# Performance work log

Hardware: AMD Instinct MI355X
Metric: run time of the kernel (lower is better)

## Reference

```python
import jax, jax.numpy as jnp
import numpy as np

B = 4096
N_PATCH = 196  # 14x14 patches of a 28x28 image
THRESHOLD = 0.9
SECONDARY = 0.5
SECONDARY_WEIGHT = 0.5

_CNOT = jnp.array([[1, 0, 0, 0], [0, 1, 0, 0], [0, 0, 0, 1], [0, 0, 1, 0]], dtype=jnp.complex64)


def _ry(t):
    c, s = jnp.cos(t / 2), jnp.sin(t / 2)
    m = jnp.stack([jnp.stack([c, -s], -1), jnp.stack([s, c], -1)], -2)
    return m.astype(jnp.complex64)


def _rx(t):
    c, s = jnp.cos(t / 2), jnp.sin(t / 2)
    z = jnp.zeros_like(c)
    re = jnp.stack([jnp.stack([c, z], -1), jnp.stack([z, c], -1)], -2)
    im = jnp.stack([jnp.stack([z, -s], -1), jnp.stack([-s, z], -1)], -2)
    return (re + 1j * im).astype(jnp.complex64)


def _rz(t):
    em = jnp.exp(-0.5j * t.astype(jnp.complex64) if hasattr(t, 'astype') else -0.5j * t)
    ep = jnp.conj(em)
    z = jnp.zeros_like(em)
    m = jnp.stack([jnp.stack([em, z], -1), jnp.stack([z, ep], -1)], -2)
    return m.astype(jnp.complex64)


def _apply_1q(state, mat, wire):
    # state: (P, 2, 2, 2, 2); mat: (2,2) shared or (P,2,2) per-sample
    s = jnp.moveaxis(state, 1 + wire, -1)
    if mat.ndim == 2:
        s = jnp.einsum('pabcj,ij->pabci', s, mat)
    else:
        s = jnp.einsum('pabcj,pij->pabci', s, mat)
    return jnp.moveaxis(s, -1, 1 + wire)


def _apply_2q(state, mat4, w0, w1):
    s = jnp.moveaxis(state, (1 + w0, 1 + w1), (-2, -1))
    shp = s.shape
    s = s.reshape(shp[:-2] + (4,))
    s = jnp.einsum('...j,ij->...i', s, mat4)
    return jnp.moveaxis(s.reshape(shp), (-2, -1), (1 + w0, 1 + w1))


def _quantum_measure(angles, q_params):
    # angles: (P, 4) real -> Pauli-Z expectations (P, 4)
    P = angles.shape[0]
    state = jnp.zeros((P, 2, 2, 2, 2), jnp.complex64).at[:, 0, 0, 0, 0].set(1.0)
    # GeneralEncoder: RY(pixel) on each wire
    for w in range(4):
        state = _apply_1q(state, _ry(angles[:, w]), w)
    # fixed 'RandomLayer' (8 ops, deterministic gate sequence, trainable params)
    state = _apply_1q(state, _rx(q_params[0]), 0)
    state = _apply_1q(state, _ry(q_params[1]), 1)
    state = _apply_1q(state, _rz(q_params[2]), 2)
    state = _apply_2q(state, _CNOT, 0, 1)
    state = _apply_1q(state, _rx(q_params[3]), 3)
    state = _apply_2q(state, _CNOT, 2, 3)
    state = _apply_1q(state, _ry(q_params[4]), 0)
    state = _apply_1q(state, _rz(q_params[5]), 3)
    probs = state.real ** 2 + state.imag ** 2
    exps = []
    for w in range(4):
        p = jnp.moveaxis(probs, 1 + w, 1)
        exps.append((p[:, 0] - p[:, 1]).reshape(P, -1).sum(-1))
    return jnp.stack(exps, -1)


def setup_inputs() -> dict:
    key = jax.random.key(0)
    k1, k2, k3, k4 = jax.random.split(key, 4)
    x = jax.random.uniform(k1, (B, 1, 28, 28), dtype=jnp.float32)
    q_params = jax.random.uniform(k2, (6,), dtype=jnp.float32) * 2.0 * np.pi
    W = jax.random.normal(k3, (10, 4 * 14 * 14), dtype=jnp.float32) * 0.03
    b = jax.random.normal(k4, (10,), dtype=jnp.float32) * 0.01
    return {"x": x, "q_params": q_params, "W": W, "b": b}


def reference(x, q_params, W, b):
    Bsz = x.shape[0]
    # extract 2x2 patches in (tl, tr, bl, br) order -> (B*196, 4)
    p = x[:, 0].reshape(Bsz, 14, 2, 14, 2)
    p = jnp.transpose(p, (0, 1, 3, 2, 4)).reshape(Bsz * N_PATCH, 4)
    meas = _quantum_measure(p, q_params).reshape(Bsz, N_PATCH, 4)
    # adjacency from cosine similarity of first sample's patch vectors
    v = meas[0]
    nrm = jnp.linalg.norm(v, axis=-1, keepdims=True)
    sim = (v @ v.T) / (nrm * nrm.T + 1e-12)
    adj = jnp.where(sim >= THRESHOLD, 1.0,
                    jnp.where(sim >= SECONDARY, SECONDARY_WEIGHT, 0.0)).astype(meas.dtype)
    agg = jnp.einsum('nm,bmd->bnd', adj, meas)
    logits = agg.reshape(Bsz, -1) @ W.T + b
    return jax.nn.log_softmax(logits, axis=-1)
```

## Files before the change

kernel.cpp:

```cpp
#include <hip/hip_runtime.h>
#include <hip/hip_bf16.h>


#define NP 196

__device__ __forceinline__ float quad3(const float* H, const float* wa,
                                       const float* wb) {
  return wa[0] * (H[0] * wb[0] + H[1] * wb[1] + H[2] * wb[2]) +
         wa[1] * (H[3] * wb[0] + H[4] * wb[1] + H[5] * wb[2]) +
         wa[2] * (H[6] * wb[0] + H[7] * wb[1] + H[8] * wb[2]);
}

__device__ __forceinline__ void build_H_all(const float* __restrict__ qp,
                                            float* __restrict__ H) {
  float qc[6], qs[6];
#pragma unroll
  for (int i = 0; i < 6; ++i) __sincosf(0.5f * qp[i], &qs[i], &qc[i]);
#pragma unroll
  for (int sub = 0; sub < 2; ++sub) {
    float Mr[4][4] = {}, Mi[4][4] = {};
    if (sub == 0) {
      Mr[0][0] = Mr[1][1] = Mr[2][2] = Mr[3][3] = qc[0];
      Mi[0][2] = Mi[2][0] = Mi[1][3] = Mi[3][1] = -qs[0];
#pragma unroll
      for (int j = 0; j < 4; ++j) {
        float a, b;
        a = Mr[0][j]; b = Mr[1][j]; Mr[0][j] = qc[1]*a - qs[1]*b; Mr[1][j] = qs[1]*a + qc[1]*b;
        a = Mi[0][j]; b = Mi[1][j]; Mi[0][j] = qc[1]*a - qs[1]*b; Mi[1][j] = qs[1]*a + qc[1]*b;
        a = Mr[2][j]; b = Mr[3][j]; Mr[2][j] = qc[1]*a - qs[1]*b; Mr[3][j] = qs[1]*a + qc[1]*b;
        a = Mi[2][j]; b = Mi[3][j]; Mi[2][j] = qc[1]*a - qs[1]*b; Mi[3][j] = qs[1]*a + qc[1]*b;
      }
#pragma unroll
      for (int j = 0; j < 4; ++j) {
        float r = Mr[2][j]; Mr[2][j] = Mr[3][j]; Mr[3][j] = r;
        float q = Mi[2][j]; Mi[2][j] = Mi[3][j]; Mi[3][j] = q;
      }
#pragma unroll
      for (int j = 0; j < 4; ++j) {
        float a, b;
        a = Mr[0][j]; b = Mr[2][j]; Mr[0][j] = qc[4]*a - qs[4]*b; Mr[2][j] = qs[4]*a + qc[4]*b;
        a = Mi[0][j]; b = Mi[2][j]; Mi[0][j] = qc[4]*a - qs[4]*b; Mi[2][j] = qs[4]*a + qc[4]*b;
        a = Mr[1][j]; b = Mr[3][j]; Mr[1][j] = qc[4]*a - qs[4]*b; Mr[3][j] = qs[4]*a + qc[4]*b;
        a = Mi[1][j]; b = Mi[3][j]; Mi[1][j] = qc[4]*a - qs[4]*b; Mi[3][j] = qs[4]*a + qc[4]*b;
      }
    } else {
      Mr[0][0] = Mr[1][1] = Mr[2][2] = Mr[3][3] = qc[2];
      Mi[0][0] = Mi[1][1] = -qs[2]; Mi[2][2] = Mi[3][3] = qs[2];
#pragma unroll
      for (int j = 0; j < 4; ++j) {
        float ra, ia, rb, ib;
        ra = Mr[0][j]; ia = Mi[0][j]; rb = Mr[1][j]; ib = Mi[1][j];
        Mr[0][j] = qc[3]*ra + qs[3]*ib;  Mi[0][j] = qc[3]*ia - qs[3]*rb;
        Mr[1][j] = qc[3]*rb + qs[3]*ia;  Mi[1][j] = qc[3]*ib - qs[3]*ra;
        ra = Mr[2][j]; ia = Mi[2][j]; rb = Mr[3][j]; ib = Mi[3][j];
        Mr[2][j] = qc[3]*ra + qs[3]*ib;  Mi[2][j] = qc[3]*ia - qs[3]*rb;
        Mr[3][j] = qc[3]*rb + qs[3]*ia;  Mi[3][j] = qc[3]*ib - qs[3]*ra;
      }
#pragma unroll
      for (int j = 0; j < 4; ++j) {
        float r = Mr[2][j]; Mr[2][j] = Mr[3][j]; Mr[3][j] = r;
        float q = Mi[2][j]; Mi[2][j] = Mi[3][j]; Mi[3][j] = q;
      }
#pragma unroll
      for (int r = 0; r < 4; ++r) {
        float sg = (r & 1) ? 1.0f : -1.0f;
#pragma unroll
        for (int j = 0; j < 4; ++j) {
          float re = Mr[r][j], im = Mi[r][j];
          Mr[r][j] = qc[5] * re - sg * qs[5] * im;
          Mi[r][j] = qc[5] * im + sg * qs[5] * re;
        }
      }
    }
#pragma unroll
    for (int d = 0; d < 2; ++d) {
      float G[4][4];
#pragma unroll
      for (int j = 0; j < 4; ++j)
#pragma unroll
        for (int k = 0; k < 4; ++k) {
          float g = 0.0f;
#pragma unroll
          for (int i = 0; i < 4; ++i) {
            float sg = (d == 0) ? ((i < 2) ? 1.f : -1.f)
                                : (((i & 1) == 0) ? 1.f : -1.f);
            g += sg * (Mr[i][j] * Mr[i][k] + Mi[i][j] * Mi[i][k]);
          }
          G[j][k] = g;
        }
      float* Hd = H + sub * 18 + d * 9;
      Hd[0] = G[0][0];       Hd[1] = 2.f * G[0][1];               Hd[2] = G[1][1];
      Hd[3] = 2.f * G[0][2]; Hd[4] = 2.f * (G[0][3] + G[1][2]);   Hd[5] = 2.f * G[1][3];
      Hd[6] = G[2][2];       Hd[7] = 2.f * G[2][3];               Hd[8] = G[3][3];
    }
  }
}

__device__ __forceinline__ void meas_patch(const float* __restrict__ xb, int p,
                                           const float* __restrict__ H,
                                           float* e) {
  int i = p / 14, j = p - 14 * i;
  float2 top = *(const float2*)(xb + 56 * i + 2 * j);
  float2 bot = *(const float2*)(xb + 56 * i + 28 + 2 * j);
  float c0, s0, c1, s1, c2, s2, c3, s3;
  __sincosf(0.5f * top.x, &s0, &c0);
  __sincosf(0.5f * top.y, &s1, &c1);
  __sincosf(0.5f * bot.x, &s2, &c2);
  __sincosf(0.5f * bot.y, &s3, &c3);
  float wA0[3] = {c0 * c0, c0 * s0, s0 * s0};
  float wA1[3] = {c1 * c1, c1 * s1, s1 * s1};
  float wB0[3] = {c2 * c2, c2 * s2, s2 * s2};
  float wB1[3] = {c3 * c3, c3 * s3, s3 * s3};
  e[0] = quad3(H, wA0, wA1);
  e[1] = quad3(H + 9, wA0, wA1);
  e[2] = quad3(H + 18, wB0, wB1);
  e[3] = quad3(H + 27, wB0, wB1);
}

__global__ __launch_bounds__(256, 1) void k_w2(const float* __restrict__ x,
                                               const float* __restrict__ qp,
                                               const float* __restrict__ W,
                                               float* __restrict__ W2,
                                               float* __restrict__ HG) {
  __shared__ float vs[NP][4];
  __shared__ float ns[NP];
  __shared__ float wrow[NP];
  __shared__ float red[160];
  int m = blockIdx.x, t = threadIdx.x;

  float H[36];
  build_H_all(qp, H);

  if (m == 0 && t == 0) {
#pragma unroll
    for (int i = 0; i < 36; ++i) HG[i] = H[i];
  }

  if (t < NP) {
    float e[4];
    meas_patch(x, t, H, e);
    vs[t][0] = e[0]; vs[t][1] = e[1]; vs[t][2] = e[2]; vs[t][3] = e[3];
    ns[t] = sqrtf(e[0]*e[0] + e[1]*e[1] + e[2]*e[2] + e[3]*e[3]);
  }
  __syncthreads();
  float v0 = vs[m][0], v1 = vs[m][1], v2 = vs[m][2], v3 = vs[m][3];
  float nm = ns[m];
  if (t < NP) {
    float dot = v0 * vs[t][0] + v1 * vs[t][1] + v2 * vs[t][2] + v3 * vs[t][3];
    float sim = dot / (nm * ns[t] + 1e-12f);
    wrow[t] = (sim >= 0.9f) ? 1.0f : ((sim >= 0.5f) ? 0.5f : 0.0f);
  }
  __syncthreads();
  if (t < 160) {
    int pair = t >> 2, chunk = t & 3;
    int k = pair >> 2, d = pair & 3;
    const float* Wk = W + k * 784 + d;
    float acc = 0.0f;
    int n0 = chunk * 49;
#pragma unroll 7
    for (int n = n0; n < n0 + 49; ++n) acc += wrow[n] * Wk[4 * n];
    red[t] = acc;
  }
  __syncthreads();
  if (t < 40) {
    int k = t >> 2, d = t & 3;
    W2[k * 784 + 4 * m + d] = red[4*t] + red[4*t+1] + red[4*t+2] + red[4*t+3];
  }
}

__global__ __launch_bounds__(256, 2) void k_main(const float* __restrict__ x,
                                                 const float* __restrict__ HG,
                                                 const float* __restrict__ bias,
                                                 const float* __restrict__ W2,
                                                 float* __restrict__ out,
                                                 int Bsz) {
  __shared__ float red[4][160];
  int t = threadIdx.x, wv = t >> 6, lane = t & 63;
  int b0 = blockIdx.x * 8 + wv * 2;
  bool vA = b0 < Bsz, vB = (b0 + 1) < Bsz;

  float H[36];
#pragma unroll
  for (int i = 0; i < 36; ++i) H[i] = HG[i];

  const float* xa = x + (size_t)b0 * 784;
  const float* xb = xa + 784;
  float accA[10], accB[10];
#pragma unroll
  for (int k = 0; k < 10; ++k) { accA[k] = 0.0f; accB[k] = 0.0f; }

#pragma unroll
  for (int r = 0; r < 4; ++r) {
    int p = lane + 64 * r;
    if (p < NP) {
      float eA[4] = {0.f, 0.f, 0.f, 0.f};
      float eB[4] = {0.f, 0.f, 0.f, 0.f};
      if (vA) meas_patch(xa, p, H, eA);
      if (vB) meas_patch(xb, p, H, eB);
#pragma unroll
      for (int k = 0; k < 10; ++k) {
        float4 w = *(const float4*)(W2 + k * 784 + 4 * p);
        accA[k] += eA[0] * w.x + eA[1] * w.y + eA[2] * w.z + eA[3] * w.w;
        accB[k] += eB[0] * w.x + eB[1] * w.y + eB[2] * w.z + eB[3] * w.w;
      }
    }
  }

#pragma unroll
  for (int k = 0; k < 10; ++k) {
#pragma unroll
    for (int off = 32; off >= 8; off >>= 1) {
      accA[k] += __shfl_xor(accA[k], off);
      accB[k] += __shfl_xor(accB[k], off);
    }
  }
  if (lane < 8) {
#pragma unroll
    for (int k = 0; k < 10; ++k) {
      red[wv][k * 8 + lane]      = accA[k];
      red[wv][80 + k * 8 + lane] = accB[k];
    }
  }
  __syncthreads();

  int s = lane >> 5;
  int k10 = lane & 31;
  float lg = -1e30f;
  if (k10 < 10) {
    const float4* q = (const float4*)&red[wv][s * 80 + k10 * 8];
    float4 a = q[0], b4 = q[1];
    lg = ((a.x + a.y) + (a.z + a.w)) + ((b4.x + b4.y) + (b4.z + b4.w)) +
         bias[k10];
  }
  float mx = lg;
#pragma unroll
  for (int off = 8; off; off >>= 1) mx = fmaxf(mx, __shfl_xor(mx, off));
  float ex = (k10 < 10) ? __expf(lg - mx) : 0.0f;
  float sm = ex;
#pragma unroll
  for (int off = 8; off; off >>= 1) sm += __shfl_xor(sm, off);
  float lse = mx + __logf(sm);
  bool vs_ = s ? vB : vA;
  if (k10 < 10 && vs_) out[(size_t)(b0 + s) * 10 + k10] = lg - lse;
}

extern "C" void kernel_launch(void* const* d_in, const int* in_sizes, int n_in,
                              void* d_out, int out_size, void* d_ws, size_t ws_size,
                              hipStream_t stream) {
  const float* x  = (const float*)d_in[0];
  const float* qp = (const float*)d_in[1];
  const float* W  = (const float*)d_in[2];
  const float* bi = (const float*)d_in[3];
  float* out = (float*)d_out;

  int Bsz = in_sizes[0] / 784;

  float* W2 = (float*)d_ws;
  float* HG = W2 + 7840;

  k_w2<<<NP, 256, 0, stream>>>(x, qp, W, W2, HG);
  k_main<<<(Bsz + 7) / 8, 256, 0, stream>>>(x, HG, bi, W2, out, Bsz);
}
```

Baseline: 77.17 us.

## Use full-angle quadratic form for patch measurement and stage W2 in LDS

Rewrites the patch measurement in terms of cos/sin of the full pixel angle. The 3x3 coefficient matrices are pre-transformed once into a basis of (cos, sin, 1), so each expectation is a few fused multiply-adds with no squared half-angle terms. k_main also copies the 31 KB W2 matrix into shared memory once per block, so the inner loop reads it from LDS instead of global memory. This cuts ALU work and global traffic per patch, at the cost of a block-wide sync and more LDS use, which may reduce occupancy.

```diff
diff --git a/kernel.cpp b/kernel.cpp
--- a/kernel.cpp
+++ b/kernel.cpp
@@ -9,6 +9,31 @@
   return wa[0] * (H[0] * wb[0] + H[1] * wb[1] + H[2] * wb[2]) +
          wa[1] * (H[3] * wb[0] + H[4] * wb[1] + H[5] * wb[2]) +
          wa[2] * (H[6] * wb[0] + H[7] * wb[1] + H[8] * wb[2]);
+}
+
+__device__ __forceinline__ float qform(const float* __restrict__ H, float Ca,
+                                       float Sa, float Cb, float Sb) {
+  float u0 = fmaf(Cb, H[0], fmaf(Sb, H[1], H[2]));
+  float u1 = fmaf(Cb, H[3], fmaf(Sb, H[4], H[5]));
+  float u2 = fmaf(Cb, H[6], fmaf(Sb, H[7], H[8]));
+  return fmaf(Ca, u0, fmaf(Sa, u1, u2));
+}
+
+__device__ __forceinline__ void xform9(const float* __restrict__ Hin,
+                                       float* __restrict__ Ho) {
+  float A[9];
+#pragma unroll
+  for (int r = 0; r < 3; ++r) {
+    A[3 * r + 0] = 0.5f * (Hin[3 * r + 0] - Hin[3 * r + 2]);
+    A[3 * r + 1] = 0.5f * Hin[3 * r + 1];
+    A[3 * r + 2] = 0.5f * (Hin[3 * r + 0] + Hin[3 * r + 2]);
+  }
+#pragma unroll
+  for (int c = 0; c < 3; ++c) {
+    Ho[0 + c] = 0.5f * (A[c] - A[6 + c]);
+    Ho[3 + c] = 0.5f * A[3 + c];
+    Ho[6 + c] = 0.5f * (A[c] + A[6 + c]);
+  }
 }
 
 __device__ __forceinline__ void build_H_all(const float* __restrict__ qp,
@@ -117,6 +142,23 @@
   e[3] = quad3(H + 27, wB0, wB1);
 }
 
+__device__ __forceinline__ void meas_patch2(const float* __restrict__ xb, int p,
+                                            const float* __restrict__ H,
+                                            float* e) {
+  int i = p / 14, j = p - 14 * i;
+  float2 top = *(const float2*)(xb + 56 * i + 2 * j);
+  float2 bot = *(const float2*)(xb + 56 * i + 28 + 2 * j);
+  float C0, S0, C1, S1, C2, S2, C3, S3;
+  __sincosf(top.x, &S0, &C0);
+  __sincosf(top.y, &S1, &C1);
+  __sincosf(bot.x, &S2, &C2);
+  __sincosf(bot.y, &S3, &C3);
+  e[0] = qform(H,      C0, S0, C1, S1);
+  e[1] = qform(H + 9,  C0, S0, C1, S1);
+  e[2] = qform(H + 18, C2, S2, C3, S3);
+  e[3] = qform(H + 27, C2, S2, C3, S3);
+}
+
 __global__ __launch_bounds__(256, 1) void k_w2(const float* __restrict__ x,
                                                const float* __restrict__ qp,
                                                const float* __restrict__ W,
@@ -132,8 +174,11 @@
   build_H_all(qp, H);
 
   if (m == 0 && t == 0) {
-#pragma unroll
-    for (int i = 0; i < 36; ++i) HG[i] = H[i];
+    float H2[36];
+#pragma unroll
+    for (int q = 0; q < 4; ++q) xform9(H + 9 * q, H2 + 9 * q);
+#pragma unroll
+    for (int i = 0; i < 36; ++i) HG[i] = H2[i];
   }
 
   if (t < NP) {
@@ -174,14 +219,26 @@
                                                  const float* __restrict__ W2,
                                                  float* __restrict__ out,
                                                  int Bsz) {
+  __shared__ __align__(16) float W2s[7840];
   __shared__ float red[4][160];
   int t = threadIdx.x, wv = t >> 6, lane = t & 63;
   int b0 = blockIdx.x * 8 + wv * 2;
   bool vA = b0 < Bsz, vB = (b0 + 1) < Bsz;
 
+  {
+    float4* dst = (float4*)W2s;
+    const float4* src = (const float4*)W2;
+#pragma unroll
+    for (int i = 0; i < 8; ++i) {
+      int idx = t + 256 * i;
+      if (idx < 1960) dst[idx] = src[idx];
+    }
+  }
+
   float H[36];
 #pragma unroll
   for (int i = 0; i < 36; ++i) H[i] = HG[i];
+  __syncthreads();
 
   const float* xa = x + (size_t)b0 * 784;
   const float* xb = xa + 784;
@@ -195,11 +252,11 @@
     if (p < NP) {
       float eA[4] = {0.f, 0.f, 0.f, 0.f};
       float eB[4] = {0.f, 0.f, 0.f, 0.f};
-      if (vA) meas_patch(xa, p, H, eA);
-      if (vB) meas_patch(xb, p, H, eB);
+      if (vA) meas_patch2(xa, p, H, eA);
+      if (vB) meas_patch2(xb, p, H, eB);
 #pragma unroll
       for (int k = 0; k < 10; ++k) {
-        float4 w = *(const float4*)(W2 + k * 784 + 4 * p);
+        float4 w = *(const float4*)(W2s + k * 784 + 4 * p);
         accA[k] += eA[0] * w.x + eA[1] * w.y + eA[2] * w.z + eA[3] * w.w;
         accB[k] += eB[0] * w.x + eB[1] * w.y + eB[2] * w.z + eB[3] * w.w;
       }
```

Result: no change. 77.73 us (+0.7%).
